# Performance work log

Hardware: AMD Instinct MI355X
Metric: run time of the kernel (lower is better)

Reference implementation:

```python
import jax, jax.numpy as jnp
import numpy as np

HEADS = 4
DIM_HEAD = 32


def setup_inputs() -> dict:
    key = jax.random.key(0)
    k1, k2, k3 = jax.random.split(key, 3)
    b, c, h, w = 2, 256, 64, 64
    hidden = HEADS * DIM_HEAD  # 128
    x = jax.random.normal(k1, (b, c, h, w), dtype=jnp.float32)
    # conv1x1 weights (out_ch, in_ch); scaled like torch default init
    w_qkv = jax.random.normal(k2, (hidden * 3, c), dtype=jnp.float32) * (1.0 / np.sqrt(c))
    w_out = jax.random.normal(k3, (c, hidden), dtype=jnp.float32) * (1.0 / np.sqrt(hidden))
    b_out = jnp.zeros((c,), dtype=jnp.float32)
    return {"x": x, "w_qkv": w_qkv, "w_out": w_out, "b_out": b_out}


def reference(x, w_qkv, w_out, b_out):
    b, c, h, w = x.shape
    hw = h * w
    scale = DIM_HEAD ** -0.5
    # 1x1 conv == channel GEMM
    qkv = jnp.einsum('oc,bchw->bohw', w_qkv, x)
    # replicate torch view(b, heads, dim_head, 3, h*w): q/k/v interleaved per channel
    qkv = qkv.reshape(b, HEADS, DIM_HEAD, 3, hw)
    q = qkv[..., 0, :] * scale           # (b, H, d, N)
    k = qkv[..., 1, :]
    v = qkv[..., 2, :]
    sim = jnp.einsum('bhdi,bhdj->bhij', q, k)   # (b, H, N, N)
    attn = jax.nn.softmax(sim, axis=-1)         # max-subtract softmax (same math)
    out = jnp.einsum('bhij,bhdj->bhid', attn, v)  # (b, H, N, d)
    out = out.transpose(0, 1, 3, 2).reshape(b, HEADS * DIM_HEAD, h, w)
    return jnp.einsum('oc,bchw->bohw', w_out, out) + b_out[None, :, None, None]
```

## Files before the change

### kernel.cpp

```cpp
#include <hip/hip_runtime.h>

#define HEADS 4
#define DIM_HEAD 32
#define NB 2
#define NC 256
#define HW 4096
#define HIDDEN 128
#define NBH (NB*HEADS)
#define ROWS_TOTAL (NBH*HW)

typedef _Float16 f16;
typedef _Float16 f16x8 __attribute__((ext_vector_type(8)));
typedef __fp16 fp16x2 __attribute__((ext_vector_type(2)));
typedef float f32x4 __attribute__((ext_vector_type(4)));

#define XT_OFF   0u
#define QT_OFF   (4u<<20)
#define KT_OFF   (6u<<20)
#define VH_OFF   (8u<<20)
#define HIDT_OFF (10u<<20)
#define WQH_OFF  (12u<<20)
#define WOH_OFF  ((12u<<20) + (256u<<10))

__device__ __forceinline__ f16x8 ldg_f16x8(const f16* p) {
    union { uint4 u; f16x8 v; } t;
    t.u = *reinterpret_cast<const uint4*>(p);
    return t.v;
}
__device__ __forceinline__ unsigned packh2(float a, float b) {
    union { fp16x2 h; unsigned u; } t;
    t.h = __builtin_amdgcn_cvt_pkrtz(a, b);
    return t.u;
}

__global__ __launch_bounds__(256) void prep(const float* __restrict__ x,
                                            const float* __restrict__ wqkv,
                                            const float* __restrict__ wout,
                                            f16* __restrict__ xt,
                                            f16* __restrict__ wqh,
                                            f16* __restrict__ woh) {
    __shared__ float T[64][65];
    if (blockIdx.x < 512) {
        const int idx = blockIdx.x;
        const int b = idx >> 8, rem = idx & 255;
        const int c0 = (rem >> 6) * 64, s0 = (rem & 63) * 64;
        const int t = threadIdx.x;
        #pragma unroll
        for (int i = 0; i < 16; ++i) {
            int e = t + i * 256;
            int c = e >> 6, s = e & 63;
            T[c][s] = x[((size_t)(b * NC + c0 + c)) * HW + s0 + s];
        }
        __syncthreads();
        const int s = t >> 2, cg = (t & 3) * 16;
        unsigned ov[8];
        #pragma unroll
        for (int i = 0; i < 8; ++i)
            ov[i] = packh2(T[cg + 2 * i][s], T[cg + 2 * i + 1][s]);
        const int srow = s0 + s;
        f16* dst = xt + ((((size_t)(b * 256 + (srow >> 4))) * 8 + ((c0 + cg) >> 5)) << 9)
                      + (srow & 15) * 32 + (cg & 31);
        *reinterpret_cast<uint4*>(dst)     = make_uint4(ov[0], ov[1], ov[2], ov[3]);
        *reinterpret_cast<uint4*>(dst + 8) = make_uint4(ov[4], ov[5], ov[6], ov[7]);
        return;
    }
    const int tid = (blockIdx.x - 512) * 256 + threadIdx.x;
    const float QSCALE = 0.17677669529663687f * 1.4426950408889634f;
    if (tid < 24576) {
        int o_lin = tid >> 6;
        int c4 = (tid & 63) * 4;
        int which = o_lin >> 7, r = o_lin & 127;
        int head = r >> 5, d = r & 31;
        int o_g = head * 96 + d * 3 + which;
        float4 v = *reinterpret_cast<const float4*>(wqkv + o_g * 256 + c4);
        float scl = (which == 0) ? QSCALE : 1.0f;
        uint2 pv;
        pv.x = packh2(v.x * scl, v.y * scl);
        pv.y = packh2(v.z * scl, v.w * scl);
        f16* dst = wqh + (((o_lin >> 4) * 8 + (c4 >> 5)) << 9)
                       + (o_lin & 15) * 32 + (c4 & 31);
        *reinterpret_cast<uint2*>(dst) = pv;
    } else if (tid < 24576 + 8192) {
        int t2 = tid - 24576;
        int o = t2 >> 5;
        int c4 = (t2 * 4) & 127;
        float4 v = *reinterpret_cast<const float4*>(wout + t2 * 4);
        uint2 pv;
        pv.x = packh2(v.x, v.y);
        pv.y = packh2(v.z, v.w);
        f16* dst = woh + (((o >> 4) * 4 + (c4 >> 5)) << 9)
                       + (o & 15) * 32 + (c4 & 31);
        *reinterpret_cast<uint2*>(dst) = pv;
    }
}

__global__ __launch_bounds__(256) void qkv_mfma(const f16* __restrict__ xt,
                                                const f16* __restrict__ wqh,
                                                f16* __restrict__ qt,
                                                f16* __restrict__ kt,
                                                f16* __restrict__ vh) {
    const int w = threadIdx.x >> 6, lane = threadIdx.x & 63;
    const int q15 = lane & 15, quad = lane >> 4;
    const int b = blockIdx.z;
    const int sTile = blockIdx.x * 64 + (w & 1) * 32;
    const int oTile = blockIdx.y * 64 + (w >> 1) * 32;
    const f16* At = xt + (((size_t)(b * 256 + (sTile >> 4))) << 12);
    const f16* Bt = wqh + (((size_t)(oTile >> 4)) << 12);
    const int fo = q15 * 32 + quad * 8;

    f32x4 acc[2][2];
    #pragma unroll
    for (int i = 0; i < 2; ++i)
        #pragma unroll
        for (int j = 0; j < 2; ++j) acc[i][j] = (f32x4){0.f, 0.f, 0.f, 0.f};

    #pragma unroll
    for (int kc = 0; kc < 256; kc += 32) {
        const int kt5 = (kc >> 5) << 9;
        f16x8 a0 = ldg_f16x8(At + kt5 + fo);
        f16x8 a1 = ldg_f16x8(At + 4096 + kt5 + fo);
        f16x8 b0 = ldg_f16x8(Bt + kt5 + fo);
        f16x8 b1 = ldg_f16x8(Bt + 4096 + kt5 + fo);
        acc[0][0] = __builtin_amdgcn_mfma_f32_16x16x32_f16(a0, b0, acc[0][0], 0, 0, 0);
        acc[0][1] = __builtin_amdgcn_mfma_f32_16x16x32_f16(a0, b1, acc[0][1], 0, 0, 0);
        acc[1][0] = __builtin_amdgcn_mfma_f32_16x16x32_f16(a1, b0, acc[1][0], 0, 0, 0);
        acc[1][1] = __builtin_amdgcn_mfma_f32_16x16x32_f16(a1, b1, acc[1][1], 0, 0, 0);
    }

    #pragma unroll
    for (int si = 0; si < 2; ++si)
        #pragma unroll
        for (int oj = 0; oj < 2; ++oj) {
            int o_lin = oTile + oj * 16 + q15;
            int which = o_lin >> 7;
            int r = o_lin & 127;
            int head = r >> 5, d = r & 31;
            int bh = b * HEADS + head;
            int s2 = sTile + si * 16 + quad * 4;
            if (which == 2) {
                uint2 pv;
                pv.x = packh2(acc[si][oj][0], acc[si][oj][1]);
                pv.y = packh2(acc[si][oj][2], acc[si][oj][3]);
                f16* dst = vh + ((((size_t)bh * 128 + (sTile >> 5)) * 32 + d) << 5)
                              + quad * 8 + si * 4;
                *reinterpret_cast<uint2*>(dst) = pv;
            } else {
                f16* dst = (which == 0 ? qt : kt) + (size_t)bh * HW * 32;
                #pragma unroll
                for (int r2 = 0; r2 < 4; ++r2)
                    dst[(size_t)(s2 + r2) * 32 + d] = (f16)acc[si][oj][r2];
            }
        }
}

#define MFMA16(A,B,C) __builtin_amdgcn_mfma_f32_16x16x32_f16(A,B,C,0,0,0)

#define LDKV(kd0,kd1,vd0,vd1,J)                                             \
    kd0 = ldg_f16x8(Kb + (size_t)((J) + q15) * 32 + quad * 8);              \
    kd1 = ldg_f16x8(Kb + (size_t)((J) + 16 + q15) * 32 + quad * 8);         \
    vd0 = ldg_f16x8(Vb + (((size_t)((J) >> 5) * 32 + q15) << 5) + quad * 8);\
    vd1 = ldg_f16x8(Vb + (((size_t)((J) >> 5) * 32 + 16 + q15) << 5) + quad * 8);

#define CHUNK(kf0_,kf1_,vf0_,vf1_)                                       \
    {                                                                    \
        const f32x4 z = {0.f, 0.f, 0.f, 0.f};                            \
        f32x4 s0a = MFMA16(kf0_, qf0, z);                                \
        f32x4 s1a = MFMA16(kf1_, qf0, z);                                \
        f32x4 s0b = MFMA16(kf0_, qf1, z);                                \
        f32x4 s1b = MFMA16(kf1_, qf1, z);                                \
        float ea[8], eb[8];                                              \
        _Pragma("unroll")                                                \
        for (int r = 0; r < 4; ++r) {                                    \
            ea[r]   = __builtin_amdgcn_exp2f(s0a[r]);                    \
            ea[4+r] = __builtin_amdgcn_exp2f(s1a[r]);                    \
            eb[r]   = __builtin_amdgcn_exp2f(s0b[r]);                    \
            eb[4+r] = __builtin_amdgcn_exp2f(s1b[r]);                    \
        }                                                                \
        l0 += (ea[0]+ea[1])+(ea[2]+ea[3])+(ea[4]+ea[5])+(ea[6]+ea[7]);   \
        l1 += (eb[0]+eb[1])+(eb[2]+eb[3])+(eb[4]+eb[5])+(eb[6]+eb[7]);   \
        union { unsigned u[4]; f16x8 v; } pa, pb;                        \
        pa.u[0] = packh2(ea[0], ea[1]); pa.u[1] = packh2(ea[2], ea[3]);  \
        pa.u[2] = packh2(ea[4], ea[5]); pa.u[3] = packh2(ea[6], ea[7]);  \
        pb.u[0] = packh2(eb[0], eb[1]); pb.u[1] = packh2(eb[2], eb[3]);  \
        pb.u[2] = packh2(eb[4], eb[5]); pb.u[3] = packh2(eb[6], eb[7]);  \
        acc[0][0] = MFMA16(vf0_, pa.v, acc[0][0]);                       \
        acc[0][1] = MFMA16(vf1_, pa.v, acc[0][1]);                       \
        acc[1][0] = MFMA16(vf0_, pb.v, acc[1][0]);                       \
        acc[1][1] = MFMA16(vf1_, pb.v, acc[1][1]);                       \
    }

__global__ __launch_bounds__(256) void attn_fused(const f16* __restrict__ qt,
                                                  const f16* __restrict__ kt,
                                                  const f16* __restrict__ vh,
                                                  f16* __restrict__ hidt) {
    __shared__ float Lo[4 * 4 * 256];
    __shared__ float Ll[4][2][16];
    const int w    = threadIdx.x >> 6;
    const int lane = threadIdx.x & 63;
    const int q15  = lane & 15;
    const int quad = lane >> 4;

    const int L    = blockIdx.x;
    const int bh   = L & 7;
    const int qblk = L >> 3;
    const int qbase = qblk * 32;

    const f16* Qb = qt + (size_t)bh * HW * 32;
    const f16* Kb = kt + (size_t)bh * HW * 32;
    const f16* Vb = vh + (size_t)bh * 128 * 1024;

    f16x8 qf0 = ldg_f16x8(Qb + (size_t)(qbase + q15) * 32 + quad * 8);
    f16x8 qf1 = ldg_f16x8(Qb + (size_t)(qbase + 16 + q15) * 32 + quad * 8);

    f32x4 acc[2][2];
    #pragma unroll
    for (int a = 0; a < 2; ++a)
        #pragma unroll
        for (int b2 = 0; b2 < 2; ++b2)
            acc[a][b2] = (f32x4){0.f, 0.f, 0.f, 0.f};
    float l0 = 0.f, l1 = 0.f;

    const int j0   = w * 1024;
    const int span = min(1024, HW - j0);

    f16x8 ka0, ka1, va0, va1, kb0, kb1, vb0, vb1;
    LDKV(ka0, ka1, va0, va1, j0);
    LDKV(kb0, kb1, vb0, vb1, j0 + 32);

    for (int jc = 0; jc < span; jc += 64) {
        CHUNK(ka0, ka1, va0, va1);
        LDKV(ka0, ka1, va0, va1, j0 + jc + 64);
        CHUNK(kb0, kb1, vb0, vb1);
        LDKV(kb0, kb1, vb0, vb1, j0 + jc + 96);
    }

    l0 += __shfl_xor(l0, 16, 64);
    l0 += __shfl_xor(l0, 32, 64);
    l1 += __shfl_xor(l1, 16, 64);
    l1 += __shfl_xor(l1, 32, 64);
    if (quad == 0) { Ll[w][0][q15] = l0; Ll[w][1][q15] = l1; }

    float* Wo = Lo + w * 1024;
    #pragma unroll
    for (int qb = 0; qb < 2; ++qb)
        #pragma unroll
        for (int t = 0; t < 2; ++t)
            *reinterpret_cast<f32x4*>(Wo + (qb * 2 + t) * 256 + lane * 4) = acc[qb][t];
    __syncthreads();

    const int row  = threadIdx.x >> 3;
    const int dg   = threadIdx.x & 7;
    const int qb   = row >> 4, q15r = row & 15;
    const int t_   = dg >> 2, quadr = dg & 3;
    const float l = Ll[0][qb][q15r] + Ll[1][qb][q15r] + Ll[2][qb][q15r] + Ll[3][qb][q15r];
    const float inv = 1.0f / l;
    float o0 = 0.f, o1 = 0.f, o2 = 0.f, o3 = 0.f;
    #pragma unroll
    for (int ww = 0; ww < 4; ++ww) {
        const float* p = Lo + ww * 1024 + (qb * 2 + t_) * 256 + (quadr * 16 + q15r) * 4;
        o0 += p[0]; o1 += p[1]; o2 += p[2]; o3 += p[3];
    }
    uint2 pv;
    pv.x = packh2(o0 * inv, o1 * inv);
    pv.y = packh2(o2 * inv, o3 * inv);
    const int s = qbase + row;
    const int b = bh >> 2, h = bh & 3;
    const int d = t_ * 16 + quadr * 4;
    f16* dst = hidt + ((((size_t)(b * 256 + (s >> 4))) * 4 + h) << 9)
                    + (s & 15) * 32 + d;
    *reinterpret_cast<uint2*>(dst) = pv;
}

__global__ __launch_bounds__(256) void outp_mfma(const f16* __restrict__ hidt,
                                                 const f16* __restrict__ woh,
                                                 const float* __restrict__ bout,
                                                 float* __restrict__ out) {
    const int w = threadIdx.x >> 6, lane = threadIdx.x & 63;
    const int q15 = lane & 15, quad = lane >> 4;
    const int b = blockIdx.z;
    const int sTile = blockIdx.x * 64 + (w & 1) * 32;
    const int oTile = blockIdx.y * 64 + (w >> 1) * 32;
    const f16* At = hidt + (((size_t)(b * 256 + (sTile >> 4))) << 11);
    const f16* Bt = woh + (((size_t)(oTile >> 4)) << 11);
    const int fo = q15 * 32 + quad * 8;

    f32x4 acc[2][2];
    #pragma unroll
    for (int i = 0; i < 2; ++i)
        #pragma unroll
        for (int j = 0; j < 2; ++j) acc[i][j] = (f32x4){0.f, 0.f, 0.f, 0.f};

    #pragma unroll
    for (int kc = 0; kc < 128; kc += 32) {
        const int kt5 = (kc >> 5) << 9;
        f16x8 a0 = ldg_f16x8(At + kt5 + fo);
        f16x8 a1 = ldg_f16x8(At + 2048 + kt5 + fo);
        f16x8 b0 = ldg_f16x8(Bt + kt5 + fo);
        f16x8 b1 = ldg_f16x8(Bt + 2048 + kt5 + fo);
        acc[0][0] = __builtin_amdgcn_mfma_f32_16x16x32_f16(a0, b0, acc[0][0], 0, 0, 0);
        acc[0][1] = __builtin_amdgcn_mfma_f32_16x16x32_f16(a0, b1, acc[0][1], 0, 0, 0);
        acc[1][0] = __builtin_amdgcn_mfma_f32_16x16x32_f16(a1, b0, acc[1][0], 0, 0, 0);
        acc[1][1] = __builtin_amdgcn_mfma_f32_16x16x32_f16(a1, b1, acc[1][1], 0, 0, 0);
    }

    #pragma unroll
    for (int oj = 0; oj < 2; ++oj) {
        const int o = oTile + oj * 16 + q15;
        const float bias = bout[o];
        #pragma unroll
        for (int si = 0; si < 2; ++si) {
            const int s2 = sTile + si * 16 + quad * 4;
            float4 v = make_float4(acc[si][oj][0] + bias, acc[si][oj][1] + bias,
                                   acc[si][oj][2] + bias, acc[si][oj][3] + bias);
            *reinterpret_cast<float4*>(out + ((size_t)(b * NC + o)) * HW + s2) = v;
        }
    }
}

extern "C" void kernel_launch(void* const* d_in, const int* in_sizes, int n_in,
                              void* d_out, int out_size, void* d_ws, size_t ws_size,
                              hipStream_t stream) {
    const float* x    = (const float*)d_in[0];
    const float* wqkv = (const float*)d_in[1];
    const float* wout = (const float*)d_in[2];
    const float* bout = (const float*)d_in[3];
    float* out = (float*)d_out;
    char* wsb  = (char*)d_ws;

    f16*   XT   = (f16*)(wsb + XT_OFF);
    f16*   QT   = (f16*)(wsb + QT_OFF);
    f16*   KT   = (f16*)(wsb + KT_OFF);
    f16*   VH   = (f16*)(wsb + VH_OFF);
    f16*   HIDT = (f16*)(wsb + HIDT_OFF);
    f16*   WQH  = (f16*)(wsb + WQH_OFF);
    f16*   WOH  = (f16*)(wsb + WOH_OFF);

    prep      <<<dim3(640), 256, 0, stream>>>(x, wqkv, wout, XT, WQH, WOH);
    qkv_mfma  <<<dim3(64, 6, NB), 256, 0, stream>>>(XT, WQH, QT, KT, VH);
    attn_fused<<<dim3(1024), 256, 0, stream>>>(QT, KT, VH, HIDT);
    outp_mfma <<<dim3(64, 4, NB), 256, 0, stream>>>(HIDT, WOH, bout, out);
}
```

Baseline: 113.6 us.

## Fuse prep transpose and weight conversion into QKV and output GEMM kernels

Removes the separate prep kernel: the QKV GEMM now loads fp32 x tiles into shared memory, transposes and converts them to fp16 fragments in-kernel, and converts fp32 weights (with q scaling) on the fly. The output projection likewise reads fp32 w_out directly and packs it to fp16 per iteration. This saves one launch and the XT round trip through global memory. In exchange, each of the 6 o-tile blocks re-reads and re-converts the same x tile, and weights are re-converted per block.

```diff
diff --git a/kernel.cpp b/kernel.cpp
--- a/kernel.cpp
+++ b/kernel.cpp
@@ -7,20 +7,18 @@
 #define HW 4096
 #define HIDDEN 128
 #define NBH (NB*HEADS)
-#define ROWS_TOTAL (NBH*HW)
 
 typedef _Float16 f16;
 typedef _Float16 f16x8 __attribute__((ext_vector_type(8)));
 typedef __fp16 fp16x2 __attribute__((ext_vector_type(2)));
 typedef float f32x4 __attribute__((ext_vector_type(4)));
 
-#define XT_OFF   0u
 #define QT_OFF   (4u<<20)
 #define KT_OFF   (6u<<20)
 #define VH_OFF   (8u<<20)
 #define HIDT_OFF (10u<<20)
-#define WQH_OFF  (12u<<20)
-#define WOH_OFF  ((12u<<20) + (256u<<10))
+
+#define QSCALE (0.17677669529663687f * 1.4426950408889634f)
 
 __device__ __forceinline__ f16x8 ldg_f16x8(const f16* p) {
     union { uint4 u; f16x8 v; } t;
@@ -33,80 +31,55 @@
     return t.u;
 }
 
-__global__ __launch_bounds__(256) void prep(const float* __restrict__ x,
-                                            const float* __restrict__ wqkv,
-                                            const float* __restrict__ wout,
-                                            f16* __restrict__ xt,
-                                            f16* __restrict__ wqh,
-                                            f16* __restrict__ woh) {
-    __shared__ float T[64][65];
-    if (blockIdx.x < 512) {
-        const int idx = blockIdx.x;
-        const int b = idx >> 8, rem = idx & 255;
-        const int c0 = (rem >> 6) * 64, s0 = (rem & 63) * 64;
-        const int t = threadIdx.x;
-        #pragma unroll
-        for (int i = 0; i < 16; ++i) {
-            int e = t + i * 256;
-            int c = e >> 6, s = e & 63;
-            T[c][s] = x[((size_t)(b * NC + c0 + c)) * HW + s0 + s];
-        }
-        __syncthreads();
-        const int s = t >> 2, cg = (t & 3) * 16;
-        unsigned ov[8];
-        #pragma unroll
-        for (int i = 0; i < 8; ++i)
-            ov[i] = packh2(T[cg + 2 * i][s], T[cg + 2 * i + 1][s]);
-        const int srow = s0 + s;
-        f16* dst = xt + ((((size_t)(b * 256 + (srow >> 4))) * 8 + ((c0 + cg) >> 5)) << 9)
-                      + (srow & 15) * 32 + (cg & 31);
-        *reinterpret_cast<uint4*>(dst)     = make_uint4(ov[0], ov[1], ov[2], ov[3]);
-        *reinterpret_cast<uint4*>(dst + 8) = make_uint4(ov[4], ov[5], ov[6], ov[7]);
-        return;
-    }
-    const int tid = (blockIdx.x - 512) * 256 + threadIdx.x;
-    const float QSCALE = 0.17677669529663687f * 1.4426950408889634f;
-    if (tid < 24576) {
-        int o_lin = tid >> 6;
-        int c4 = (tid & 63) * 4;
-        int which = o_lin >> 7, r = o_lin & 127;
-        int head = r >> 5, d = r & 31;
-        int o_g = head * 96 + d * 3 + which;
-        float4 v = *reinterpret_cast<const float4*>(wqkv + o_g * 256 + c4);
-        float scl = (which == 0) ? QSCALE : 1.0f;
-        uint2 pv;
-        pv.x = packh2(v.x * scl, v.y * scl);
-        pv.y = packh2(v.z * scl, v.w * scl);
-        f16* dst = wqh + (((o_lin >> 4) * 8 + (c4 >> 5)) << 9)
-                       + (o_lin & 15) * 32 + (c4 & 31);
-        *reinterpret_cast<uint2*>(dst) = pv;
-    } else if (tid < 24576 + 8192) {
-        int t2 = tid - 24576;
-        int o = t2 >> 5;
-        int c4 = (t2 * 4) & 127;
-        float4 v = *reinterpret_cast<const float4*>(wout + t2 * 4);
-        uint2 pv;
-        pv.x = packh2(v.x, v.y);
-        pv.y = packh2(v.z, v.w);
-        f16* dst = woh + (((o >> 4) * 4 + (c4 >> 5)) << 9)
-                       + (o & 15) * 32 + (c4 & 31);
-        *reinterpret_cast<uint2*>(dst) = pv;
-    }
-}
-
-__global__ __launch_bounds__(256) void qkv_mfma(const f16* __restrict__ xt,
-                                                const f16* __restrict__ wqh,
+#define MFMA16(A,B,C) __builtin_amdgcn_mfma_f32_16x16x32_f16(A,B,C,0,0,0)
+
+__global__ __launch_bounds__(256) void qkv_mfma(const float* __restrict__ x,
+                                                const float* __restrict__ wqkv,
                                                 f16* __restrict__ qt,
                                                 f16* __restrict__ kt,
                                                 f16* __restrict__ vh) {
+    __shared__ float T[64][65];
     const int w = threadIdx.x >> 6, lane = threadIdx.x & 63;
     const int q15 = lane & 15, quad = lane >> 4;
     const int b = blockIdx.z;
-    const int sTile = blockIdx.x * 64 + (w & 1) * 32;
+    const int s0g = blockIdx.x * 64;
+    const int sTile = s0g + (w & 1) * 32;
     const int oTile = blockIdx.y * 64 + (w >> 1) * 32;
-    const f16* At = xt + (((size_t)(b * 256 + (sTile >> 4))) << 12);
-    const f16* Bt = wqh + (((size_t)(oTile >> 4)) << 12);
-    const int fo = q15 * 32 + quad * 8;
+
+    f16x8 a[8][2];
+    #pragma unroll
+    for (int cc = 0; cc < 256; cc += 64) {
+        if (cc) __syncthreads();
+        #pragma unroll
+        for (int i = 0; i < 16; ++i) {
+            int e = threadIdx.x + i * 256;
+            int c = e >> 6, s = e & 63;
+            T[c][s] = x[((size_t)(b * NC + cc + c)) * HW + s0g + s];
+        }
+        __syncthreads();
+        #pragma unroll
+        for (int ktl = 0; ktl < 2; ++ktl)
+            #pragma unroll
+            for (int h = 0; h < 2; ++h) {
+                const int sl = (w & 1) * 32 + h * 16 + q15;
+                const int cb = ktl * 32 + quad * 8;
+                union { unsigned u[4]; f16x8 v; } t;
+                #pragma unroll
+                for (int j = 0; j < 4; ++j)
+                    t.u[j] = packh2(T[cb + 2 * j][sl], T[cb + 2 * j + 1][sl]);
+                a[(cc >> 5) + ktl][h] = t.v;
+            }
+    }
+
+    const int o0 = oTile + q15, o1 = oTile + 16 + q15;
+    const int wh0 = o0 >> 7, r0 = o0 & 127;
+    const int og0 = (r0 >> 5) * 96 + (r0 & 31) * 3 + wh0;
+    const int wh1 = o1 >> 7, r1 = o1 & 127;
+    const int og1 = (r1 >> 5) * 96 + (r1 & 31) * 3 + wh1;
+    const float scl0 = (wh0 == 0) ? QSCALE : 1.0f;
+    const float scl1 = (wh1 == 0) ? QSCALE : 1.0f;
+    const float* W0 = wqkv + og0 * 256 + quad * 8;
+    const float* W1 = wqkv + og1 * 256 + quad * 8;
 
     f32x4 acc[2][2];
     #pragma unroll
@@ -115,16 +88,24 @@
         for (int j = 0; j < 2; ++j) acc[i][j] = (f32x4){0.f, 0.f, 0.f, 0.f};
 
     #pragma unroll
-    for (int kc = 0; kc < 256; kc += 32) {
-        const int kt5 = (kc >> 5) << 9;
-        f16x8 a0 = ldg_f16x8(At + kt5 + fo);
-        f16x8 a1 = ldg_f16x8(At + 4096 + kt5 + fo);
-        f16x8 b0 = ldg_f16x8(Bt + kt5 + fo);
-        f16x8 b1 = ldg_f16x8(Bt + 4096 + kt5 + fo);
-        acc[0][0] = __builtin_amdgcn_mfma_f32_16x16x32_f16(a0, b0, acc[0][0], 0, 0, 0);
-        acc[0][1] = __builtin_amdgcn_mfma_f32_16x16x32_f16(a0, b1, acc[0][1], 0, 0, 0);
-        acc[1][0] = __builtin_amdgcn_mfma_f32_16x16x32_f16(a1, b0, acc[1][0], 0, 0, 0);
-        acc[1][1] = __builtin_amdgcn_mfma_f32_16x16x32_f16(a1, b1, acc[1][1], 0, 0, 0);
+    for (int kt = 0; kt < 8; ++kt) {
+        float4 p0 = *reinterpret_cast<const float4*>(W0 + kt * 32);
+        float4 p1 = *reinterpret_cast<const float4*>(W0 + kt * 32 + 4);
+        float4 r0v = *reinterpret_cast<const float4*>(W1 + kt * 32);
+        float4 r1v = *reinterpret_cast<const float4*>(W1 + kt * 32 + 4);
+        union { unsigned u[4]; f16x8 v; } b0, b1;
+        b0.u[0] = packh2(p0.x * scl0, p0.y * scl0);
+        b0.u[1] = packh2(p0.z * scl0, p0.w * scl0);
+        b0.u[2] = packh2(p1.x * scl0, p1.y * scl0);
+        b0.u[3] = packh2(p1.z * scl0, p1.w * scl0);
+        b1.u[0] = packh2(r0v.x * scl1, r0v.y * scl1);
+        b1.u[1] = packh2(r0v.z * scl1, r0v.w * scl1);
+        b1.u[2] = packh2(r1v.x * scl1, r1v.y * scl1);
+        b1.u[3] = packh2(r1v.z * scl1, r1v.w * scl1);
+        acc[0][0] = MFMA16(a[kt][0], b0.v, acc[0][0]);
+        acc[0][1] = MFMA16(a[kt][0], b1.v, acc[0][1]);
+        acc[1][0] = MFMA16(a[kt][1], b0.v, acc[1][0]);
+        acc[1][1] = MFMA16(a[kt][1], b1.v, acc[1][1]);
     }
 
     #pragma unroll
@@ -152,8 +133,6 @@
             }
         }
 }
-
-#define MFMA16(A,B,C) __builtin_amdgcn_mfma_f32_16x16x32_f16(A,B,C,0,0,0)
 
 #define LDKV(kd0,kd1,vd0,vd1,J)                                             \
     kd0 = ldg_f16x8(Kb + (size_t)((J) + q15) * 32 + quad * 8);              \
@@ -272,7 +251,7 @@
 }
 
 __global__ __launch_bounds__(256) void outp_mfma(const f16* __restrict__ hidt,
-                                                 const f16* __restrict__ woh,
+                                                 const float* __restrict__ wout,
                                                  const float* __restrict__ bout,
                                                  float* __restrict__ out) {
     const int w = threadIdx.x >> 6, lane = threadIdx.x & 63;
@@ -281,8 +260,9 @@
     const int sTile = blockIdx.x * 64 + (w & 1) * 32;
     const int oTile = blockIdx.y * 64 + (w >> 1) * 32;
     const f16* At = hidt + (((size_t)(b * 256 + (sTile >> 4))) << 11);
-    const f16* Bt = woh + (((size_t)(oTile >> 4)) << 11);
     const int fo = q15 * 32 + quad * 8;
+    const float* W0 = wout + (oTile + q15) * 128 + quad * 8;
+    const float* W1 = wout + (oTile + 16 + q15) * 128 + quad * 8;
 
     f32x4 acc[2][2];
     #pragma unroll
@@ -291,16 +271,22 @@
         for (int j = 0; j < 2; ++j) acc[i][j] = (f32x4){0.f, 0.f, 0.f, 0.f};
 
     #pragma unroll
-    for (int kc = 0; kc < 128; kc += 32) {
-        const int kt5 = (kc >> 5) << 9;
-        f16x8 a0 = ldg_f16x8(At + kt5 + fo);
-        f16x8 a1 = ldg_f16x8(At + 2048 + kt5 + fo);
-        f16x8 b0 = ldg_f16x8(Bt + kt5 + fo);
-        f16x8 b1 = ldg_f16x8(Bt + 2048 + kt5 + fo);
-        acc[0][0] = __builtin_amdgcn_mfma_f32_16x16x32_f16(a0, b0, acc[0][0], 0, 0, 0);
-        acc[0][1] = __builtin_amdgcn_mfma_f32_16x16x32_f16(a0, b1, acc[0][1], 0, 0, 0);
-        acc[1][0] = __builtin_amdgcn_mfma_f32_16x16x32_f16(a1, b0, acc[1][0], 0, 0, 0);
-        acc[1][1] = __builtin_amdgcn_mfma_f32_16x16x32_f16(a1, b1, acc[1][1], 0, 0, 0);
+    for (int kt = 0; kt < 4; ++kt) {
+        f16x8 a0 = ldg_f16x8(At + kt * 512 + fo);
+        f16x8 a1 = ldg_f16x8(At + 2048 + kt * 512 + fo);
+        float4 p0 = *reinterpret_cast<const float4*>(W0 + kt * 32);
+        float4 p1 = *reinterpret_cast<const float4*>(W0 + kt * 32 + 4);
+        float4 r0v = *reinterpret_cast<const float4*>(W1 + kt * 32);
+        float4 r1v = *reinterpret_cast<const float4*>(W1 + kt * 32 + 4);
+        union { unsigned u[4]; f16x8 v; } b0, b1;
+        b0.u[0] = packh2(p0.x, p0.y);  b0.u[1] = packh2(p0.z, p0.w);
+        b0.u[2] = packh2(p1.x, p1.y);  b0.u[3] = packh2(p1.z, p1.w);
+        b1.u[0] = packh2(r0v.x, r0v.y); b1.u[1] = packh2(r0v.z, r0v.w);
+        b1.u[2] = packh2(r1v.x, r1v.y); b1.u[3] = packh2(r1v.z, r1v.w);
+        acc[0][0] = MFMA16(a0, b0.v, acc[0][0]);
+        acc[0][1] = MFMA16(a0, b1.v, acc[0][1]);
+        acc[1][0] = MFMA16(a1, b0.v, acc[1][0]);
+        acc[1][1] = MFMA16(a1, b1.v, acc[1][1]);
     }
 
     #pragma unroll
@@ -327,16 +313,12 @@
     float* out = (float*)d_out;
     char* wsb  = (char*)d_ws;
 
-    f16*   XT   = (f16*)(wsb + XT_OFF);
     f16*   QT   = (f16*)(wsb + QT_OFF);
     f16*   KT   = (f16*)(wsb + KT_OFF);
     f16*   VH   = (f16*)(wsb + VH_OFF);
     f16*   HIDT = (f16*)(wsb + HIDT_OFF);
-    f16*   WQH  = (f16*)(wsb + WQH_OFF);
-    f16*   WOH  = (f16*)(wsb + WOH_OFF);
-
-    prep      <<<dim3(640), 256, 0, stream>>>(x, wqkv, wout, XT, WQH, WOH);
-    qkv_mfma  <<<dim3(64, 6, NB), 256, 0, stream>>>(XT, WQH, QT, KT, VH);
+
+    qkv_mfma  <<<dim3(64, 6, NB), 256, 0, stream>>>(x, wqkv, QT, KT, VH);
     attn_fused<<<dim3(1024), 256, 0, stream>>>(QT, KT, VH, HIDT);
-    outp_mfma <<<dim3(64, 4, NB), 256, 0, stream>>>(HIDT, WOH, bout, out);
-}
+    outp_mfma <<<dim3(64, 4, NB), 256, 0, stream>>>(HIDT, wout, bout, out);
+}
```

Result: slower. 121.8 us (+7.3%).
